# Kernel tuning notes

Hardware: AMD Instinct MI355X
Metric: run time of the kernel (lower is better)

## Reference

```python
import jax, jax.numpy as jnp
import numpy as np

B, S, D, H = 4, 2048, 512, 8
HD = D // H  # head dim = 64
NEG = 1e9


def setup_inputs() -> dict:
    key = jax.random.key(0)
    ks = jax.random.split(key, 10)
    x = jax.random.normal(ks[0], (B, S, D), dtype=jnp.float32)
    group_ids = jnp.sort(jax.random.randint(ks[1], (B, S), 0, 8), axis=-1)
    s = 0.05
    Wq = jax.random.normal(ks[2], (D, D), dtype=jnp.float32) * s
    Wk = jax.random.normal(ks[3], (D, D), dtype=jnp.float32) * s
    Wv = jax.random.normal(ks[4], (D, D), dtype=jnp.float32) * s
    Wo = jax.random.normal(ks[5], (D, D), dtype=jnp.float32) * s
    bq = jnp.zeros((D,), jnp.float32)
    bk = jnp.zeros((D,), jnp.float32)
    bv = jnp.zeros((D,), jnp.float32)
    bo = jnp.zeros((D,), jnp.float32)
    return {"x": x, "group_ids": group_ids, "Wq": Wq, "bq": bq,
            "Wk": Wk, "bk": bk, "Wv": Wv, "bv": bv, "Wo": Wo, "bo": bo}


def reference(x, group_ids, Wq, bq, Wk, bk, Wv, bv, Wo, bo):
    relu = jax.nn.relu
    # projections + activation (activation='relu' is applied to q,k,v AND output)
    q = relu(x @ Wq + bq)  # [B,S,D]
    k = relu(x @ Wk + bk)
    v = relu(x @ Wv + bv)
    # split heads -> [B,H,S,HD]
    def split(t):
        return t.reshape(B, S, H, HD).transpose(0, 2, 1, 3)
    qh, kh, vh = split(q), split(k), split(v)
    # note: scale uses feature dim AFTER head split, i.e. head_dim
    scale = 1.0 / jnp.sqrt(jnp.float32(HD))
    e = jnp.einsum('bhqd,bhkd->bhqk', qh, kh) * scale  # [B,H,S,S]
    group_mask = (group_ids[:, None, :, None] == group_ids[:, None, None, :])  # [B,1,S,S]
    e = e - (1.0 - group_mask.astype(jnp.float32)) * NEG
    a = jax.nn.softmax(e, axis=-1)
    yh = jnp.einsum('bhqk,bhkd->bhqd', a, vh)  # [B,H,S,HD]
    y = yh.transpose(0, 2, 1, 3).reshape(B, S, D)
    return relu(y @ Wo + bo)
```

## Files before the change

### kernel.cpp

```cpp
#include <hip/hip_runtime.h>
#include <cmath>

#define Bsz 4
#define Ssz 2048
#define Dsz 512
#define Hn 8

typedef unsigned short u16;
typedef _Float16 f16;
typedef __attribute__((ext_vector_type(4))) _Float16 f16x4;
typedef __attribute__((ext_vector_type(8))) _Float16 f16x8;
typedef __attribute__((ext_vector_type(8))) unsigned short us8;
typedef __attribute__((ext_vector_type(4))) float f32x4;
typedef __attribute__((ext_vector_type(16))) float f32x16;

__device__ __forceinline__ void gl2lds16(const void* g, void* l) {
    __builtin_amdgcn_global_load_lds(
        (const __attribute__((address_space(1))) void*)g,
        (__attribute__((address_space(3))) void*)l, 16, 0, 0);
}

__global__ __launch_bounds__(256) void prep(const float* __restrict__ x,
                                            f16* __restrict__ xb,
                                            const float* __restrict__ Wq,
                                            const float* __restrict__ Wk,
                                            const float* __restrict__ Wv,
                                            const float* __restrict__ Wo,
                                            f16* __restrict__ Wtqkv,
                                            f16* __restrict__ Wto) {
    const int blk = blockIdx.x;
    const int tid = threadIdx.x;
    if (blk < 2048) {
        int i = blk * 256 + tid;
        const float4* xv = (const float4*)x;
        float4 a = xv[2 * i], b = xv[2 * i + 1];
        f16x8 o;
        o[0] = (f16)a.x; o[1] = (f16)a.y; o[2] = (f16)a.z; o[3] = (f16)a.w;
        o[4] = (f16)b.x; o[5] = (f16)b.y; o[6] = (f16)b.z; o[7] = (f16)b.w;
        ((f16x8*)xb)[i] = o;
        return;
    }
    __shared__ float T[64][65];
    const int bz = blk - 2048;
    const int z = bz >> 6;
    const int n0 = (bz & 7) * 64, k0 = ((bz >> 3) & 7) * 64;
    const float* W = (z == 0) ? Wq : (z == 1) ? Wk : (z == 2) ? Wv : Wo;
#pragma unroll
    for (int i = 0; i < 16; i++) {
        int e = tid + i * 256;
        int r = e >> 6, c = e & 63;
        T[r][c] = W[(size_t)(k0 + r) * Dsz + n0 + c];
    }
    __syncthreads();
    f16* dst = (z < 3) ? (Wtqkv + ((size_t)z * 512 + n0) * Dsz + k0)
                       : (Wto + (size_t)n0 * Dsz + k0);
#pragma unroll
    for (int i = 0; i < 16; i++) {
        int e = tid + i * 256;
        int r = e >> 6, c = e & 63;
        dst[(size_t)r * Dsz + c] = (f16)(T[c][r]);
    }
}

template <int MODE>
__global__ __launch_bounds__(256) void gemm128(
    const f16* __restrict__ A, const f16* __restrict__ Bt,
    f16* o0, f16* o1, u16* o2v,
    const float* b0, const float* b1, const float* b2,
    float* ofp, const float* bias_f) {
    __shared__ __align__(16) u16 smem[2 * 128 * 64];
    u16* As = smem;
    u16* Bs = smem + 128 * 64;
    const int tid = threadIdx.x;
    const int colg0 = blockIdx.x * 128;
    const int row0 = blockIdx.y * 128;
    const int w = tid >> 6, lane = tid & 63;
    const int nn = lane & 31, hh = lane >> 5;
    const int wr = w >> 1, wc = w & 1;

    f32x16 acc[2][2];
#pragma unroll
    for (int bi = 0; bi < 2; bi++)
#pragma unroll
        for (int bj = 0; bj < 2; bj++)
#pragma unroll
            for (int e = 0; e < 16; e++) acc[bi][bj][e] = 0.f;

    const f16* Ablk = A + (size_t)row0 * 512;
    const f16* Bblk = Bt + (size_t)colg0 * 512;

    for (int k0 = 0; k0 < 512; k0 += 64) {
        __syncthreads();
#pragma unroll
        for (int i = 0; i < 4; i++) {
            int p = tid + i * 256;
            int m = p >> 3, kc = p & 7;
            int gk = ((kc ^ (m & 7)) << 3);
            gl2lds16(Ablk + (size_t)m * 512 + k0 + gk, As + p * 8);
            gl2lds16(Bblk + (size_t)m * 512 + k0 + gk, Bs + p * 8);
        }
        __syncthreads();
#pragma unroll
        for (int t = 0; t < 4; t++) {
            f16x8 af[2], bfr[2];
#pragma unroll
            for (int bi = 0; bi < 2; bi++) {
                int r = wr * 64 + bi * 32 + nn;
                int ch = r * 8 + ((t * 2 + hh) ^ (r & 7));
                af[bi] = *(const f16x8*)(As + ch * 8);
            }
#pragma unroll
            for (int bj = 0; bj < 2; bj++) {
                int n = wc * 64 + bj * 32 + nn;
                int ch = n * 8 + ((t * 2 + hh) ^ (n & 7));
                bfr[bj] = *(const f16x8*)(Bs + ch * 8);
            }
#pragma unroll
            for (int bi = 0; bi < 2; bi++)
#pragma unroll
                for (int bj = 0; bj < 2; bj++)
                    acc[bi][bj] = __builtin_amdgcn_mfma_f32_32x32x16_f16(
                        af[bi], bfr[bj], acc[bi][bj], 0, 0, 0);
        }
    }

    if (MODE == 0) {
        const int sel = colg0 >> 9;
        const int c0 = colg0 & 511;
        if (sel < 2) {
            f16* outp = (sel == 0) ? o0 : o1;
            const float* bp = (sel == 0) ? b0 : b1;
            const float sc = (sel == 0) ? 0.125f : 1.0f;
#pragma unroll
            for (int bj = 0; bj < 2; bj++) {
                int col = c0 + wc * 64 + bj * 32 + nn;
                float bv = bp[col];
#pragma unroll
                for (int bi = 0; bi < 2; bi++)
#pragma unroll
                    for (int rg = 0; rg < 16; rg++) {
                        int row = row0 + wr * 64 + bi * 32 +
                                  (rg & 3) + 8 * (rg >> 2) + 4 * hh;
                        outp[(size_t)row * 512 + col] =
                            (f16)(fmaxf(acc[bi][bj][rg] + bv, 0.f) * sc);
                    }
            }
        } else {
            const int hh_head = c0 >> 6;
            f16 (*T)[136] = (f16(*)[136])smem;
            const int bb = row0 >> 11;
            const int t0 = (row0 & 2047) >> 6;
            __syncthreads();
#pragma unroll
            for (int ph = 0; ph < 2; ph++) {
                if (wc == ph) {
#pragma unroll
                    for (int bj = 0; bj < 2; bj++) {
                        int d = bj * 32 + nn;
                        float bv = b2[c0 + ph * 64 + d];
#pragma unroll
                        for (int bi = 0; bi < 2; bi++)
#pragma unroll
                            for (int rg = 0; rg < 16; rg++) {
                                int s = wr * 64 + bi * 32 +
                                        (rg & 3) + 8 * (rg >> 2) + 4 * hh;
                                T[d][s] = (f16)fmaxf(acc[bi][bj][rg] + bv, 0.f);
                            }
                    }
                }
                __syncthreads();
#pragma unroll
                for (int ii = 0; ii < 4; ii++) {
                    int oct = tid + ii * 256;
                    int tt = oct >> 9, rem = oct & 511;
                    int d = rem >> 3, s8 = rem & 7;
                    us8 val = *(const us8*)(&T[d][tt * 64 + s8 * 8]);
                    size_t dst = (((size_t)((bb * 8 + hh_head + ph) * 32 + t0 + tt)) << 12)
                                 + d * 64 + s8 * 8;
                    *(us8*)(o2v + dst) = val;
                }
                __syncthreads();
            }
        }
    } else {
#pragma unroll
        for (int bj = 0; bj < 2; bj++) {
            int col = colg0 + wc * 64 + bj * 32 + nn;
            float bv = bias_f[col];
#pragma unroll
            for (int bi = 0; bi < 2; bi++)
#pragma unroll
                for (int rg = 0; rg < 16; rg++) {
                    int row = row0 + wr * 64 + bi * 32 +
                              (rg & 3) + 8 * (rg >> 2) + 4 * hh;
                    ofp[(size_t)row * 512 + col] = fmaxf(acc[bi][bj][rg] + bv, 0.f);
                }
        }
    }
}

__global__ __launch_bounds__(512) void attn_mfma(
    const f16* __restrict__ Q, const f16* __restrict__ K,
    const u16* __restrict__ VT, const int* __restrict__ G,
    f16* __restrict__ Y) {
    __shared__ __align__(16) u16 Ks[2][4096];
    __shared__ __align__(16) u16 Vs[2][4096];
    __shared__ int bnd[9];

    const int qt = blockIdx.x, h = blockIdx.y, b = blockIdx.z;
    const int q0 = qt * 128;
    const int tid = threadIdx.x;
    const int w = tid >> 6, lane = tid & 63;
    const int ln = lane & 15, quad = lane >> 4;

    const f16* Qb = Q + (size_t)b * Ssz * Dsz;
    const f16* Kb = K + (size_t)b * Ssz * Dsz;
    const u16* Vtb = VT + (size_t)(b * Hn + h) * 32 * 4096;
    const int* Gb = G + (size_t)b * Ssz;

    if (tid < 9) bnd[tid] = Ssz;
    __syncthreads();
    {
        int i0 = tid * 4;
        int4 gi = *(const int4*)(Gb + i0);
        int gp = (i0 == 0) ? -1 : Gb[i0 - 1];
        int ga[5] = {gp, gi.x, gi.y, gi.z, gi.w};
#pragma unroll
        for (int j = 0; j < 4; j++)
            for (int g = ga[j] + 1; g <= ga[j + 1]; g++) bnd[g] = i0 + j;
    }

    f16x8 qf[2];
    {
        const f16* qrow = Qb + (size_t)(q0 + w * 16 + ln) * Dsz + h * 64;
        qf[0] = *(const f16x8*)(qrow + quad * 8);
        qf[1] = *(const f16x8*)(qrow + 32 + quad * 8);
    }
    const int gq = Gb[q0 + w * 16 + ln];
    const int gqmin = Gb[q0], gqmax = Gb[q0 + 127];

    int gf = 0, gl = 0; bool ov = false;
    if (lane < 32) {
        gf = Gb[lane * 64]; gl = Gb[lane * 64 + 63];
        ov = (gl >= gqmin) && (gf <= gqmax);
    }
    unsigned long long mask = __ballot(ov);
    const int kt_lo = __builtin_ctzll(mask);
    const int kt_hi = 63 - __builtin_clzll(mask);

    __syncthreads();
    const int sq = bnd[gq];
    const unsigned usz = (unsigned)(bnd[gq + 1] - sq);

    f32x4 o[4];
    const f32x4 z4 = {0.f, 0.f, 0.f, 0.f};
#pragma unroll
    for (int nd = 0; nd < 4; nd++) o[nd] = z4;
    float lsum = 0.f;

#define STAGE_K(kt, bi_)                                                       \
    {                                                                          \
        const f16* Ktile = Kb + (size_t)(kt) * 64 * Dsz + h * 64;              \
        int row = tid >> 3, c = tid & 7;                                       \
        gl2lds16(Ktile + (size_t)row * Dsz + ((c ^ (row & 7)) << 3),           \
                 Ks[bi_] + tid * 8);                                           \
    }
#define STAGE_V(kt, bi_)                                                       \
    {                                                                          \
        const u16* Vtile = Vtb + (size_t)(kt) * 4096;                          \
        int row = tid >> 3, c = tid & 7;                                       \
        gl2lds16(Vtile + row * 64 + ((c ^ (row & 7)) << 3),                    \
                 Vs[bi_] + tid * 8);                                           \
    }

    STAGE_K(kt_lo, 0)
    STAGE_V(kt_lo, 0)

    int buf = 0;
    for (int kt = kt_lo; kt <= kt_hi; kt++) {
        __syncthreads();
        if (kt < kt_hi) { STAGE_K(kt + 1, buf ^ 1) STAGE_V(kt + 1, buf ^ 1) }
        const u16* ks = Ks[buf];
        const u16* vs = Vs[buf];
        const int k0 = kt * 64;

        f16x4 pf[4];
#pragma unroll
        for (int kb = 0; kb < 4; kb++) {
            f32x4 s = z4;
#pragma unroll
            for (int kk = 0; kk < 2; kk++) {
                int key = kb * 16 + ln;
                int ch = key * 8 + ((kk * 4 + quad) ^ (key & 7));
                f16x8 kf = *(const f16x8*)(ks + ch * 8);
                s = __builtin_amdgcn_mfma_f32_16x16x32_f16(kf, qf[kk], s, 0, 0, 0);
            }
            const int ckb = k0 + kb * 16 + quad * 4;
            f16x4 pp;
#pragma unroll
            for (int r = 0; r < 4; r++) {
                float t = s[r] - 4.0f;
                float sval = ((unsigned)(ckb + r - sq) < usz) ? t : -1e9f;
                float e = __expf(sval);
                lsum += e;
                pp[r] = (f16)e;
            }
            pf[kb] = pp;
        }
#pragma unroll
        for (int nd = 0; nd < 4; nd++)
#pragma unroll
            for (int kc = 0; kc < 4; kc++) {
                int addr = (((nd * 16 + ln) * 8 +
                             ((kc * 2 + (quad >> 1)) ^ (ln & 7))) << 3) +
                           (quad & 1) * 4;
                f16x4 vf = *(const f16x4*)(vs + addr);
                o[nd] = __builtin_amdgcn_mfma_f32_16x16x16f16(pf[kc], vf, o[nd], 0, 0, 0);
            }
        buf ^= 1;
    }

    lsum += __shfl_xor(lsum, 16);
    lsum += __shfl_xor(lsum, 32);
    float linv = 1.0f / lsum;
#pragma unroll
    for (int r = 0; r < 4; r++) {
        float lr = __shfl(linv, (lane & 48) | (quad * 4 + r));
        size_t row = (size_t)b * Ssz + q0 + w * 16 + quad * 4 + r;
#pragma unroll
        for (int nd = 0; nd < 4; nd++)
            Y[row * Dsz + h * 64 + nd * 16 + ln] = (f16)(o[nd][r] * lr);
    }
#undef STAGE_K
#undef STAGE_V
}

extern "C" void kernel_launch(void* const* d_in, const int* in_sizes, int n_in,
                              void* d_out, int out_size, void* d_ws, size_t ws_size,
                              hipStream_t stream) {
    const float* x  = (const float*)d_in[0];
    const int*   g  = (const int*)d_in[1];
    const float* Wq = (const float*)d_in[2];
    const float* bq = (const float*)d_in[3];
    const float* Wk = (const float*)d_in[4];
    const float* bk = (const float*)d_in[5];
    const float* Wv = (const float*)d_in[6];
    const float* bv = (const float*)d_in[7];
    const float* Wo = (const float*)d_in[8];
    const float* bo = (const float*)d_in[9];
    float* out = (float*)d_out;

    const size_t E = (size_t)Bsz * Ssz * Dsz;
    f16* xb  = (f16*)d_ws;
    f16* qb  = xb + E;
    f16* kb2 = qb + E;
    u16* vtb = (u16*)(kb2 + E);
    f16* yb  = (f16*)(vtb + E);
    f16* Wtqkv = yb + E;
    f16* Wto   = Wtqkv + 1536 * 512;

    prep<<<2304, 256, 0, stream>>>(x, xb, Wq, Wk, Wv, Wo, Wtqkv, Wto);
    gemm128<0><<<dim3(12, 64), 256, 0, stream>>>(xb, Wtqkv, qb, kb2, vtb,
                                                 bq, bk, bv, nullptr, nullptr);
    attn_mfma<<<dim3(Ssz / 128, Hn, Bsz), 512, 0, stream>>>(qb, kb2, vtb, g, yb);
    gemm128<1><<<dim3(4, 64), 256, 0, stream>>>(yb, Wto, nullptr, nullptr, nullptr,
                                                nullptr, nullptr, nullptr, out, bo);
}
```

Before: 147.1 us.

## Fuse prep, QKV GEMM, attention and output GEMM into one persistent kernel

Replaces the four separate launches with a single persistent kernel of 512 blocks. Stages are separated by a software grid barrier built from atomics on global counters, and the old kernels become device functions. Each 512-thread block runs two 128x128 GEMM tiles side by side, with each half using its own slice of shared memory. The aim is to remove launch gaps and tail effects between stages. In exchange it depends on all 512 blocks being resident at once for the barrier to work, leaves idle threads during the output GEMM, and adds barrier latency.

Result: slower. 474.5 us (+222.6%).

```diff
diff --git a/kernel.cpp b/kernel.cpp
--- a/kernel.cpp
+++ b/kernel.cpp
@@ -5,6 +5,7 @@
 #define Ssz 2048
 #define Dsz 512
 #define Hn 8
+#define NBLK 512
 
 typedef unsigned short u16;
 typedef _Float16 f16;
@@ -20,61 +21,44 @@
         (__attribute__((address_space(3))) void*)l, 16, 0, 0);
 }
 
-__global__ __launch_bounds__(256) void prep(const float* __restrict__ x,
-                                            f16* __restrict__ xb,
-                                            const float* __restrict__ Wq,
-                                            const float* __restrict__ Wk,
-                                            const float* __restrict__ Wv,
-                                            const float* __restrict__ Wo,
-                                            f16* __restrict__ Wtqkv,
-                                            f16* __restrict__ Wto) {
-    const int blk = blockIdx.x;
-    const int tid = threadIdx.x;
-    if (blk < 2048) {
-        int i = blk * 256 + tid;
-        const float4* xv = (const float4*)x;
-        float4 a = xv[2 * i], b = xv[2 * i + 1];
-        f16x8 o;
-        o[0] = (f16)a.x; o[1] = (f16)a.y; o[2] = (f16)a.z; o[3] = (f16)a.w;
-        o[4] = (f16)b.x; o[5] = (f16)b.y; o[6] = (f16)b.z; o[7] = (f16)b.w;
-        ((f16x8*)xb)[i] = o;
-        return;
-    }
-    __shared__ float T[64][65];
-    const int bz = blk - 2048;
-    const int z = bz >> 6;
-    const int n0 = (bz & 7) * 64, k0 = ((bz >> 3) & 7) * 64;
-    const float* W = (z == 0) ? Wq : (z == 1) ? Wk : (z == 2) ? Wv : Wo;
-#pragma unroll
-    for (int i = 0; i < 16; i++) {
-        int e = tid + i * 256;
-        int r = e >> 6, c = e & 63;
-        T[r][c] = W[(size_t)(k0 + r) * Dsz + n0 + c];
-    }
+__device__ int g_cnt = 0;
+__device__ int g_gen = 0;
+
+__device__ __forceinline__ void grid_barrier() {
     __syncthreads();
-    f16* dst = (z < 3) ? (Wtqkv + ((size_t)z * 512 + n0) * Dsz + k0)
-                       : (Wto + (size_t)n0 * Dsz + k0);
-#pragma unroll
-    for (int i = 0; i < 16; i++) {
-        int e = tid + i * 256;
-        int r = e >> 6, c = e & 63;
-        dst[(size_t)r * Dsz + c] = (f16)(T[c][r]);
-    }
+    if (threadIdx.x == 0) {
+        __threadfence();
+        int gseen = __hip_atomic_load(&g_gen, __ATOMIC_RELAXED,
+                                      __HIP_MEMORY_SCOPE_AGENT);
+        int a = __hip_atomic_fetch_add(&g_cnt, 1, __ATOMIC_ACQ_REL,
+                                       __HIP_MEMORY_SCOPE_AGENT);
+        if (a == NBLK - 1) {
+            __hip_atomic_store(&g_cnt, 0, __ATOMIC_RELAXED,
+                               __HIP_MEMORY_SCOPE_AGENT);
+            __hip_atomic_fetch_add(&g_gen, 1, __ATOMIC_RELEASE,
+                                   __HIP_MEMORY_SCOPE_AGENT);
+        } else {
+            while (__hip_atomic_load(&g_gen, __ATOMIC_ACQUIRE,
+                                     __HIP_MEMORY_SCOPE_AGENT) == gseen)
+                __builtin_amdgcn_s_sleep(1);
+        }
+        __threadfence();
+    }
+    __syncthreads();
 }
 
 template <int MODE>
-__global__ __launch_bounds__(256) void gemm128(
+__device__ __forceinline__ void gemm_tile(
+    const int htid, const int vcol, const int rb, u16* halfsm,
     const f16* __restrict__ A, const f16* __restrict__ Bt,
     f16* o0, f16* o1, u16* o2v,
     const float* b0, const float* b1, const float* b2,
     float* ofp, const float* bias_f) {
-    __shared__ __align__(16) u16 smem[2 * 128 * 64];
-    u16* As = smem;
-    u16* Bs = smem + 128 * 64;
-    const int tid = threadIdx.x;
-    const int colg0 = blockIdx.x * 128;
-    const int row0 = blockIdx.y * 128;
-    const int w = tid >> 6, lane = tid & 63;
+    u16* As = halfsm;
+    u16* Bs = halfsm + 128 * 64;
+    const int colg0 = vcol * 128;
+    const int row0 = rb * 128;
+    const int w = htid >> 6, lane = htid & 63;
     const int nn = lane & 31, hh = lane >> 5;
     const int wr = w >> 1, wc = w & 1;
 
@@ -93,7 +77,7 @@
         __syncthreads();
 #pragma unroll
         for (int i = 0; i < 4; i++) {
-            int p = tid + i * 256;
+            int p = htid + i * 256;
             int m = p >> 3, kc = p & 7;
             int gk = ((kc ^ (m & 7)) << 3);
             gl2lds16(Ablk + (size_t)m * 512 + k0 + gk, As + p * 8);
@@ -147,7 +131,7 @@
             }
         } else {
             const int hh_head = c0 >> 6;
-            f16 (*T)[136] = (f16(*)[136])smem;
+            f16 (*T)[136] = (f16(*)[136])halfsm;
             const int bb = row0 >> 11;
             const int t0 = (row0 & 2047) >> 6;
             __syncthreads();
@@ -171,7 +155,7 @@
                 __syncthreads();
 #pragma unroll
                 for (int ii = 0; ii < 4; ii++) {
-                    int oct = tid + ii * 256;
+                    int oct = htid + ii * 256;
                     int tt = oct >> 9, rem = oct & 511;
                     int d = rem >> 3, s8 = rem & 7;
                     us8 val = *(const us8*)(&T[d][tt * 64 + s8 * 8]);
@@ -199,15 +183,15 @@
     }
 }
 
-__global__ __launch_bounds__(512) void attn_mfma(
+__device__ __forceinline__ void attn_block(
+    const int qt, const int h, const int b, unsigned char* sm,
     const f16* __restrict__ Q, const f16* __restrict__ K,
     const u16* __restrict__ VT, const int* __restrict__ G,
     f16* __restrict__ Y) {
-    __shared__ __align__(16) u16 Ks[2][4096];
-    __shared__ __align__(16) u16 Vs[2][4096];
-    __shared__ int bnd[9];
-
-    const int qt = blockIdx.x, h = blockIdx.y, b = blockIdx.z;
+    u16 (*Ks)[4096] = (u16(*)[4096])sm;
+    u16 (*Vs)[4096] = (u16(*)[4096])(sm + 16384);
+    int* bnd = (int*)(sm + 32768);
+
     const int q0 = qt * 128;
     const int tid = threadIdx.x;
     const int w = tid >> 6, lane = tid & 63;
@@ -333,6 +317,77 @@
     }
 #undef STAGE_K
 #undef STAGE_V
+}
+
+__global__ __launch_bounds__(512, 4) void mega(
+    const float* __restrict__ x, const int* __restrict__ gids,
+    const float* __restrict__ Wq, const float* __restrict__ bq,
+    const float* __restrict__ Wk, const float* __restrict__ bk,
+    const float* __restrict__ Wv, const float* __restrict__ bv,
+    const float* __restrict__ Wo, const float* __restrict__ bo,
+    float* __restrict__ out,
+    f16* xb, f16* qb, f16* kb2, u16* vtb, f16* yb,
+    f16* Wtqkv, f16* Wto) {
+    __shared__ __align__(16) unsigned char sm[65536];
+    const int blk = blockIdx.x;
+    const int tid = threadIdx.x;
+
+    {
+        const float4* xv = (const float4*)x;
+#pragma unroll
+        for (int r = 0; r < 2; r++) {
+            int i = blk * 512 + tid + r * (NBLK * 512);
+            float4 a = xv[2 * i], b = xv[2 * i + 1];
+            f16x8 o;
+            o[0] = (f16)a.x; o[1] = (f16)a.y; o[2] = (f16)a.z; o[3] = (f16)a.w;
+            o[4] = (f16)b.x; o[5] = (f16)b.y; o[6] = (f16)b.z; o[7] = (f16)b.w;
+            ((f16x8*)xb)[i] = o;
+        }
+        if (blk < 256) {
+            float (*T)[65] = (float(*)[65])sm;
+            const int z = blk >> 6;
+            const int n0 = (blk & 7) * 64, k0 = ((blk >> 3) & 7) * 64;
+            const float* W = (z == 0) ? Wq : (z == 1) ? Wk : (z == 2) ? Wv : Wo;
+#pragma unroll
+            for (int i = 0; i < 8; i++) {
+                int e = tid + i * 512;
+                int r = e >> 6, c = e & 63;
+                T[r][c] = W[(size_t)(k0 + r) * Dsz + n0 + c];
+            }
+            __syncthreads();
+            f16* dst = (z < 3) ? (Wtqkv + ((size_t)z * 512 + n0) * Dsz + k0)
+                               : (Wto + (size_t)n0 * Dsz + k0);
+#pragma unroll
+            for (int i = 0; i < 8; i++) {
+                int e = tid + i * 512;
+                int r = e >> 6, c = e & 63;
+                dst[(size_t)r * Dsz + c] = (f16)(T[c][r]);
+            }
+        }
+    }
+    grid_barrier();
+
+    if (blk < 384) {
+        const int hw = tid >> 8, htid = tid & 255;
+        const int vcol = blk % 12, rb = (blk / 12) * 2 + hw;
+        gemm_tile<0>(htid, vcol, rb, (u16*)(sm + hw * 32768),
+                     xb, Wtqkv, qb, kb2, vtb, bq, bk, bv, nullptr, nullptr);
+    }
+    grid_barrier();
+
+    attn_block(blk & 15, (blk >> 4) & 7, blk >> 7, sm, qb, kb2, vtb, gids, yb);
+    grid_barrier();
+
+    if (blk < 256) {
+        const int hw = tid >> 8, htid = tid & 255;
+        if (hw == 0) {
+            gemm_tile<1>(htid, blk % 4, blk / 4, (u16*)sm,
+                         yb, Wto, nullptr, nullptr, nullptr,
+                         nullptr, nullptr, nullptr, out, bo);
+        } else {
+            for (int k0 = 0; k0 < 512; k0 += 64) { __syncthreads(); __syncthreads(); }
+        }
+    }
 }
 
 extern "C" void kernel_launch(void* const* d_in, const int* in_sizes, int n_in,
@@ -359,10 +414,6 @@
     f16* Wtqkv = yb + E;
     f16* Wto   = Wtqkv + 1536 * 512;
 
-    prep<<<2304, 256, 0, stream>>>(x, xb, Wq, Wk, Wv, Wo, Wtqkv, Wto);
-    gemm128<0><<<dim3(12, 64), 256, 0, stream>>>(xb, Wtqkv, qb, kb2, vtb,
-                                                 bq, bk, bv, nullptr, nullptr);
-    attn_mfma<<<dim3(Ssz / 128, Hn, Bsz), 512, 0, stream>>>(qb, kb2, vtb, g, yb);
-    gemm128<1><<<dim3(4, 64), 256, 0, stream>>>(yb, Wto, nullptr, nullptr, nullptr,
-                                                nullptr, nullptr, nullptr, out, bo);
-}
+    mega<<<NBLK, 512, 0, stream>>>(x, g, Wq, bq, Wk, bk, Wv, bv, Wo, bo,
+                                   out, xb, qb, kb2, vtb, yb, Wtqkv, Wto);
+}
```

## Fuse output projection into attention kernel via last-block-per-row-tile counter

Applied to the files above, without the earlier changes.

Removes the separate output-projection GEMM launch. Each attention block bumps an atomic counter for its 128-row tile. The last of the 8 head blocks to finish then computes the full 128x512 output tile with MFMA, reusing the attention shared memory. The counter is zeroed in the prep kernel, and launch bounds are tightened to raise occupancy. In exchange, the final GEMM runs on only 64 blocks serialized behind attention tails, and it depends on memory-fence correctness for the Y data written by other blocks.

Result: slower. 203.4 us (+38.3%).

```diff
diff --git a/kernel.cpp b/kernel.cpp
--- a/kernel.cpp
+++ b/kernel.cpp
@@ -27,10 +27,14 @@
                                             const float* __restrict__ Wv,
                                             const float* __restrict__ Wo,
                                             f16* __restrict__ Wtqkv,
-                                            f16* __restrict__ Wto) {
+                                            f16* __restrict__ Wto,
+                                            int* __restrict__ cnt) {
     const int blk = blockIdx.x;
     const int tid = threadIdx.x;
     if (blk < 2048) {
+        if (blk == 0 && tid < 64)
+            __hip_atomic_store(&cnt[tid], 0, __ATOMIC_RELAXED,
+                               __HIP_MEMORY_SCOPE_AGENT);
         int i = blk * 256 + tid;
         const float4* xv = (const float4*)x;
         float4 a = xv[2 * i], b = xv[2 * i + 1];
@@ -199,13 +203,17 @@
     }
 }
 
-__global__ __launch_bounds__(512) void attn_mfma(
+__global__ __launch_bounds__(512, 4) void attn_mfma(
     const f16* __restrict__ Q, const f16* __restrict__ K,
     const u16* __restrict__ VT, const int* __restrict__ G,
-    f16* __restrict__ Y) {
-    __shared__ __align__(16) u16 Ks[2][4096];
-    __shared__ __align__(16) u16 Vs[2][4096];
+    f16* __restrict__ Y,
+    const f16* __restrict__ Wto, const float* __restrict__ bo,
+    float* __restrict__ out, int* __restrict__ cnt) {
+    __shared__ __align__(16) u16 sm[16384];
     __shared__ int bnd[9];
+    __shared__ int finflag;
+    u16* Ksb = sm;
+    u16* Vsb = sm + 8192;
 
     const int qt = blockIdx.x, h = blockIdx.y, b = blockIdx.z;
     const int q0 = qt * 128;
@@ -263,14 +271,14 @@
         const f16* Ktile = Kb + (size_t)(kt) * 64 * Dsz + h * 64;              \
         int row = tid >> 3, c = tid & 7;                                       \
         gl2lds16(Ktile + (size_t)row * Dsz + ((c ^ (row & 7)) << 3),           \
-                 Ks[bi_] + tid * 8);                                           \
+                 Ksb + (bi_) * 4096 + tid * 8);                                \
     }
 #define STAGE_V(kt, bi_)                                                       \
     {                                                                          \
         const u16* Vtile = Vtb + (size_t)(kt) * 4096;                          \
         int row = tid >> 3, c = tid & 7;                                       \
         gl2lds16(Vtile + row * 64 + ((c ^ (row & 7)) << 3),                    \
-                 Vs[bi_] + tid * 8);                                           \
+                 Vsb + (bi_) * 4096 + tid * 8);                                \
     }
 
     STAGE_K(kt_lo, 0)
@@ -280,8 +288,8 @@
     for (int kt = kt_lo; kt <= kt_hi; kt++) {
         __syncthreads();
         if (kt < kt_hi) { STAGE_K(kt + 1, buf ^ 1) STAGE_V(kt + 1, buf ^ 1) }
-        const u16* ks = Ks[buf];
-        const u16* vs = Vs[buf];
+        const u16* ks = Ksb + buf * 4096;
+        const u16* vs = Vsb + buf * 4096;
         const int k0 = kt * 64;
 
         f16x4 pf[4];
@@ -333,6 +341,75 @@
     }
 #undef STAGE_K
 #undef STAGE_V
+
+    __syncthreads();
+    const int rb = b * 16 + qt;
+    if (tid == 0) {
+        __threadfence();
+        int old = __hip_atomic_fetch_add(&cnt[rb], 1, __ATOMIC_ACQ_REL,
+                                         __HIP_MEMORY_SCOPE_AGENT);
+        finflag = (old == 7);
+        if (old == 7) __threadfence();
+    }
+    __syncthreads();
+    if (!finflag) return;
+
+    {
+        u16* As = sm;
+        u16* Bs = sm + 8192;
+        const int nn = lane & 31, hh = lane >> 5;
+        const int wr = w >> 2, wc = w & 3;
+        const f16* Ablk = Y + (size_t)(rb * 128) * 512;
+
+        for (int vcol = 0; vcol < 4; vcol++) {
+            const f16* Bblk = Wto + (size_t)(vcol * 128) * 512;
+            f32x16 acc[2];
+#pragma unroll
+            for (int e = 0; e < 16; e++) { acc[0][e] = 0.f; acc[1][e] = 0.f; }
+
+            for (int k0 = 0; k0 < 512; k0 += 64) {
+                __syncthreads();
+#pragma unroll
+                for (int i = 0; i < 2; i++) {
+                    int p = tid + i * 512;
+                    int m = p >> 3, kc = p & 7;
+                    int gk = ((kc ^ (m & 7)) << 3);
+                    gl2lds16(Ablk + (size_t)m * 512 + k0 + gk, As + p * 8);
+                    gl2lds16(Bblk + (size_t)m * 512 + k0 + gk, Bs + p * 8);
+                }
+                __syncthreads();
+#pragma unroll
+                for (int t = 0; t < 4; t++) {
+                    f16x8 af[2], bfr;
+#pragma unroll
+                    for (int bi = 0; bi < 2; bi++) {
+                        int r = wr * 64 + bi * 32 + nn;
+                        int ch = r * 8 + ((t * 2 + hh) ^ (r & 7));
+                        af[bi] = *(const f16x8*)(As + ch * 8);
+                    }
+                    {
+                        int n = wc * 32 + nn;
+                        int ch = n * 8 + ((t * 2 + hh) ^ (n & 7));
+                        bfr = *(const f16x8*)(Bs + ch * 8);
+                    }
+                    acc[0] = __builtin_amdgcn_mfma_f32_32x32x16_f16(
+                        af[0], bfr, acc[0], 0, 0, 0);
+                    acc[1] = __builtin_amdgcn_mfma_f32_32x32x16_f16(
+                        af[1], bfr, acc[1], 0, 0, 0);
+                }
+            }
+            int col = vcol * 128 + wc * 32 + nn;
+            float bv = bo[col];
+#pragma unroll
+            for (int bi = 0; bi < 2; bi++)
+#pragma unroll
+                for (int rg = 0; rg < 16; rg++) {
+                    int row = rb * 128 + wr * 64 + bi * 32 +
+                              (rg & 3) + 8 * (rg >> 2) + 4 * hh;
+                    out[(size_t)row * 512 + col] = fmaxf(acc[bi][rg] + bv, 0.f);
+                }
+        }
+    }
 }
 
 extern "C" void kernel_launch(void* const* d_in, const int* in_sizes, int n_in,
@@ -358,11 +435,11 @@
     f16* yb  = (f16*)(vtb + E);
     f16* Wtqkv = yb + E;
     f16* Wto   = Wtqkv + 1536 * 512;
-
-    prep<<<2304, 256, 0, stream>>>(x, xb, Wq, Wk, Wv, Wo, Wtqkv, Wto);
+    int* cnt   = (int*)(Wto + 512 * 512);
+
+    prep<<<2304, 256, 0, stream>>>(x, xb, Wq, Wk, Wv, Wo, Wtqkv, Wto, cnt);
     gemm128<0><<<dim3(12, 64), 256, 0, stream>>>(xb, Wtqkv, qb, kb2, vtb,
                                                  bq, bk, bv, nullptr, nullptr);
-    attn_mfma<<<dim3(Ssz / 128, Hn, Bsz), 512, 0, stream>>>(qb, kb2, vtb, g, yb);
-    gemm128<1><<<dim3(4, 64), 256, 0, stream>>>(yb, Wto, nullptr, nullptr, nullptr,
-                                                nullptr, nullptr, nullptr, out, bo);
+    attn_mfma<<<dim3(Ssz / 128, Hn, Bsz), 512, 0, stream>>>(
+        qb, kb2, vtb, g, yb, Wto, bo, out, cnt);
 }
```
